# Kernel optimization log

Hardware: AMD Instinct MI355X
Metric: run time of the kernel (lower is better)

## Reference

```python
import jax, jax.numpy as jnp
import numpy as np

N, E, F_IN, H, D, HID, G = 50000, 800000, 64, 4, 32, 128, 1024
NEG_SLOPE = 0.2


def setup_inputs():
    key = jax.random.key(0)
    ks = jax.random.split(key, 32)
    inp = {
        "x": jax.random.normal(ks[0], (N, F_IN), dtype=jnp.float32),
        "edge_index": jax.random.randint(ks[1], (2, E), 0, N, dtype=jnp.int64),
        "batch": jnp.sort(jax.random.randint(ks[2], (N,), 0, G, dtype=jnp.int64)),
    }
    dims = [F_IN, HID, HID]
    i = 3
    for l, din in enumerate(dims):
        s = 1.0 / np.sqrt(din)
        inp[f"Wl{l}"] = jax.random.normal(ks[i], (din, H * D), dtype=jnp.float32) * s; i += 1
        inp[f"bl{l}"] = jnp.zeros((H * D,), dtype=jnp.float32)
        inp[f"Wr{l}"] = jax.random.normal(ks[i], (din, H * D), dtype=jnp.float32) * s; i += 1
        inp[f"br{l}"] = jnp.zeros((H * D,), dtype=jnp.float32)
        inp[f"att{l}"] = jax.random.normal(ks[i], (H, D), dtype=jnp.float32) * (1.0 / np.sqrt(D)); i += 1
        inp[f"b{l}"] = jnp.zeros((H * D,), dtype=jnp.float32)
    inp["Wh"] = jax.random.normal(ks[i], (HID, 1), dtype=jnp.float32) * (1.0 / np.sqrt(HID))
    inp["bh"] = jnp.zeros((1,), dtype=jnp.float32)
    return inp


def gatv2_layer(x, src, dst, Wl, bl, Wr, br, att, b):
    # GATv2Conv (eval mode, no dropout): e_ij = att . leaky_relu(Wl x_j + Wr x_i)
    xl = (x @ Wl + bl).reshape(-1, H, D)   # source transform
    xr = (x @ Wr + br).reshape(-1, H, D)   # target transform
    m = xl[src] + xr[dst]                  # [E,H,D]
    e = jnp.where(m >= 0, m, NEG_SLOPE * m)
    score = jnp.einsum("ehd,hd->eh", e, att)          # [E,H]
    smax = jax.ops.segment_max(score, dst, num_segments=N)  # [N,H]
    expv = jnp.exp(score - smax[dst])
    denom = jax.ops.segment_sum(expv, dst, num_segments=N)
    alpha = expv / denom[dst]                          # softmax over in-edges of dst
    agg = jax.ops.segment_sum(alpha[:, :, None] * xl[src], dst, num_segments=N)
    return agg.reshape(-1, H * D) + b


def reference(x, edge_index, batch, Wl0, bl0, Wr0, br0, att0, b0,
              Wl1, bl1, Wr1, br1, att1, b1,
              Wl2, bl2, Wr2, br2, att2, b2, Wh, bh):
    src, dst = edge_index[0], edge_index[1]
    params = [(Wl0, bl0, Wr0, br0, att0, b0),
              (Wl1, bl1, Wr1, br1, att1, b1),
              (Wl2, bl2, Wr2, br2, att2, b2)]
    h = x
    for p in params:
        h = gatv2_layer(h, src, dst, *p)
        h = jax.nn.elu(h)  # dropout inactive in eval
    # global mean pool over graphs
    sums = jax.ops.segment_sum(h, batch, num_segments=G)
    cnt = jax.ops.segment_sum(jnp.ones((h.shape[0],), h.dtype), batch, num_segments=G)
    pooled = sums / jnp.maximum(cnt, 1.0)[:, None]
    return pooled @ Wh + bh
```

## Files before the change

kernel.cpp:

```cpp
#include <hip/hip_runtime.h>
#include <hip/hip_fp16.h>
#include <math.h>

#define N_NODES 50000
#define N_EDGES 800000
#define HD 128
#define GG 1024
#define NEG_SLOPE 0.2f
#define SCAN_B 1024
#define NB ((N_NODES + SCAN_B - 1) / SCAN_B)

typedef __attribute__((ext_vector_type(8))) short bf16x8;
typedef __attribute__((ext_vector_type(4))) float f32x4;

__device__ __forceinline__ unsigned short f2bf(float v) {
    unsigned u = __float_as_uint(v);
    u += 0x7fff + ((u >> 16) & 1);
    return (unsigned short)(u >> 16);
}
__device__ __forceinline__ float bf2f(unsigned short s) {
    return __uint_as_float((unsigned)s << 16);
}
__device__ __forceinline__ void h8_to_f(const uint4& r, float4& v0, float4& v1) {
    const __half2* h = (const __half2*)&r;
    float2 a = __half22float2(h[0]), b = __half22float2(h[1]);
    float2 c = __half22float2(h[2]), d = __half22float2(h[3]);
    v0 = make_float4(a.x, a.y, b.x, b.y);
    v1 = make_float4(c.x, c.y, d.x, d.y);
}

__global__ void convert_x(const float* __restrict__ x, unsigned short* __restrict__ Xh,
                          unsigned short* __restrict__ Xl, int total)
{
    int i = blockIdx.x * 256 + threadIdx.x;
    if (i >= total) return;
    float v = x[i];
    unsigned short hi = f2bf(v);
    unsigned short lo = f2bf(v - bf2f(hi));
    Xh[i] = hi; Xl[i] = lo;
}

__global__ void convert_w_all(const float* __restrict__ W0l, const float* __restrict__ W0r,
                              const float* __restrict__ W1l, const float* __restrict__ W1r,
                              const float* __restrict__ W2l, const float* __restrict__ W2r,
                              unsigned short* __restrict__ Wth, unsigned short* __restrict__ Wtl)
{
    int t = blockIdx.x * 256 + threadIdx.x;
    if (t >= 256 * 64 + 2 * 256 * 128) return;
    int l, local, K;
    const float* Wl; const float* Wr;
    if (t < 256 * 64)            { l = 0; local = t;              K = 64;  Wl = W0l; Wr = W0r; }
    else if (t < 256 * 64 + 256 * 128) { l = 1; local = t - 256 * 64;  K = 128; Wl = W1l; Wr = W1r; }
    else                         { l = 2; local = t - 256 * 64 - 256 * 128; K = 128; Wl = W2l; Wr = W2r; }
    int c = local / K, k = local - c * K;
    float v = (c < 128) ? Wl[(size_t)k * 128 + c] : Wr[(size_t)k * 128 + (c - 128)];
    unsigned short hi = f2bf(v);
    unsigned short lo = f2bf(v - bf2f(hi));
    Wth[l * 256 * 128 + local] = hi;
    Wtl[l * 256 * 128 + local] = lo;
}

template<int K>
__launch_bounds__(256)
__global__ void gemm_mfma(const unsigned short* __restrict__ Xh, const unsigned short* __restrict__ Xl,
                          const unsigned short* __restrict__ Wth, const unsigned short* __restrict__ Wtl,
                          const float* __restrict__ bl, const float* __restrict__ br,
                          __half* __restrict__ Cl16, float* __restrict__ Cr, int n)
{
    constexpr int NCH = K / 32;
    const int tid  = threadIdx.x;
    const int wave = tid >> 6;
    const int lane = tid & 63;
    const int quad = lane >> 4;
    const int l15  = lane & 15;
    const int row0 = blockIdx.x * 64;

    f32x4 acc[4][4];
    #pragma unroll
    for (int i = 0; i < 4; i++)
        #pragma unroll
        for (int j = 0; j < 4; j++) acc[i][j] = (f32x4){0.f, 0.f, 0.f, 0.f};

    size_t aoff[4];
    #pragma unroll
    for (int mt = 0; mt < 4; mt++) {
        int r = row0 + mt * 16 + l15;
        if (r >= n) r = n - 1;
        aoff[mt] = (size_t)r * K + quad * 8;
    }
    size_t boff[4];
    #pragma unroll
    for (int nt = 0; nt < 4; nt++)
        boff[nt] = (size_t)(wave * 64 + nt * 16 + l15) * K + quad * 8;

    bf16x8 ah[4], al[4], bh[4], bo[4];
    #pragma unroll
    for (int mt = 0; mt < 4; mt++) {
        ah[mt] = *(const bf16x8*)(Xh + aoff[mt]);
        al[mt] = *(const bf16x8*)(Xl + aoff[mt]);
    }
    #pragma unroll
    for (int nt = 0; nt < 4; nt++) {
        bh[nt] = *(const bf16x8*)(Wth + boff[nt]);
        bo[nt] = *(const bf16x8*)(Wtl + boff[nt]);
    }

    #pragma unroll
    for (int ch = 1; ch <= NCH; ch++) {
        bf16x8 nah[4], nal[4], nbh[4], nbo[4];
        if (ch < NCH) {
            const int ko = ch * 32;
            #pragma unroll
            for (int mt = 0; mt < 4; mt++) {
                nah[mt] = *(const bf16x8*)(Xh + aoff[mt] + ko);
                nal[mt] = *(const bf16x8*)(Xl + aoff[mt] + ko);
            }
            #pragma unroll
            for (int nt = 0; nt < 4; nt++) {
                nbh[nt] = *(const bf16x8*)(Wth + boff[nt] + ko);
                nbo[nt] = *(const bf16x8*)(Wtl + boff[nt] + ko);
            }
        }
        #pragma unroll
        for (int nt = 0; nt < 4; nt++) {
            #pragma unroll
            for (int mt = 0; mt < 4; mt++) {
                acc[mt][nt] = __builtin_amdgcn_mfma_f32_16x16x32_bf16(ah[mt], bh[nt], acc[mt][nt], 0, 0, 0);
                acc[mt][nt] = __builtin_amdgcn_mfma_f32_16x16x32_bf16(ah[mt], bo[nt], acc[mt][nt], 0, 0, 0);
                acc[mt][nt] = __builtin_amdgcn_mfma_f32_16x16x32_bf16(al[mt], bh[nt], acc[mt][nt], 0, 0, 0);
            }
        }
        if (ch < NCH) {
            #pragma unroll
            for (int i = 0; i < 4; i++) {
                ah[i] = nah[i]; al[i] = nal[i];
                bh[i] = nbh[i]; bo[i] = nbo[i];
            }
        }
    }

    const bool isL = (wave < 2);
    const int colbase = (wave & 1) * 64;
    const float* bias = isL ? bl : br;
    #pragma unroll
    for (int nt = 0; nt < 4; nt++) {
        const int col = colbase + nt * 16 + l15;
        const float bv = bias[col];
        #pragma unroll
        for (int mt = 0; mt < 4; mt++) {
            #pragma unroll
            for (int r = 0; r < 4; r++) {
                const int row = row0 + mt * 16 + quad * 4 + r;
                if (row < n) {
                    const float v = acc[mt][nt][r] + bv;
                    if (isL) Cl16[(size_t)row * 128 + col] = __float2half_rn(v);
                    else     Cr  [(size_t)row * 128 + col] = v;
                }
            }
        }
    }
}

__global__ void deg_gptr(const int* __restrict__ dst, int* __restrict__ deg,
                         const int* __restrict__ batch, int* __restrict__ gptr)
{
    int i = blockIdx.x * 256 + threadIdx.x;
    if (i < N_EDGES) atomicAdd(&deg[dst[i]], 1);
    if (i <= N_NODES) {
        if (i == 0) {
            for (int g = 0; g <= batch[0]; g++) gptr[g] = 0;
        } else if (i == N_NODES) {
            for (int g = batch[N_NODES - 1] + 1; g <= GG; g++) gptr[g] = N_NODES;
        } else {
            int b0 = batch[i - 1], b1 = batch[i];
            for (int g = b0 + 1; g <= b1; g++) gptr[g] = i;
        }
    }
}

__launch_bounds__(SCAN_B)
__global__ void scan_block(const int* __restrict__ deg, int* __restrict__ rowptr,
                           int* __restrict__ btot)
{
    __shared__ int s[SCAN_B];
    const int tid = threadIdx.x;
    const int i = blockIdx.x * SCAN_B + tid;
    int v = (i < N_NODES) ? deg[i] : 0;
    s[tid] = v;
    __syncthreads();
    for (int off = 1; off < SCAN_B; off <<= 1) {
        int t = (tid >= off) ? s[tid - off] : 0;
        __syncthreads();
        s[tid] += t;
        __syncthreads();
    }
    if (i < N_NODES) rowptr[i] = s[tid] - v;
    if (tid == SCAN_B - 1) btot[blockIdx.x] = s[SCAN_B - 1];
}

__global__ void scan_btot(const int* __restrict__ btot, int* __restrict__ boff) {
    const int t = threadIdx.x;
    int v = (t < NB) ? btot[t] : 0;
    const int orig = v;
    #pragma unroll
    for (int off = 1; off < 64; off <<= 1) {
        int u = __shfl_up(v, off);
        if (t >= off) v += u;
    }
    if (t < NB) boff[t] = v - orig;
    if (t == NB - 1) boff[NB] = v;
}

__global__ void scan_add(const int* __restrict__ boff, int* __restrict__ rowptr,
                         int* __restrict__ cursor)
{
    int i = blockIdx.x * 256 + threadIdx.x;
    if (i < N_NODES) {
        int r = rowptr[i] + boff[i >> 10];
        rowptr[i] = r;
        cursor[i] = r;
    }
    if (i == N_NODES) rowptr[N_NODES] = boff[NB];
}

__global__ void scatter_csr(const int* __restrict__ src, const int* __restrict__ dst,
                            int* __restrict__ cursor, int* __restrict__ csr_src)
{
    int e = blockIdx.x * 256 + threadIdx.x;
    if (e >= N_EDGES) return;
    int pos = atomicAdd(&cursor[dst[e]], 1);
    csr_src[pos] = src[e];
}

__launch_bounds__(256)
__global__ void node_attn(const __half* __restrict__ xl16, const float* __restrict__ xr,
                          const int* __restrict__ rowptr, const int* __restrict__ csr_src,
                          const float* __restrict__ att, const float* __restrict__ bvec,
                          unsigned short* __restrict__ Hh, unsigned short* __restrict__ Hl)
{
    const int node = (blockIdx.x * 256 + threadIdx.x) >> 6;
    const int lane = threadIdx.x & 63;
    if (node >= N_NODES) return;
    const int eslot = lane >> 4;
    const int li    = lane & 15;

    const float* xrp = xr + (size_t)node * HD + li * 8;
    const float4 xr0 = *(const float4*)(xrp);
    const float4 xr1 = *(const float4*)(xrp + 4);
    const float4 aw0 = *(const float4*)(att + li * 8);
    const float4 aw1 = *(const float4*)(att + li * 8 + 4);
    const int beg = rowptr[node];
    const int end = rowptr[node + 1];

    float m = -1e30f, l = 0.f;
    float4 a0 = make_float4(0.f, 0.f, 0.f, 0.f);
    float4 a1 = make_float4(0.f, 0.f, 0.f, 0.f);

    int i0 = beg + eslot;
    int s0 = (i0 < end) ? csr_src[i0] : 0;
    uint4 cur = *(const uint4*)(xl16 + (size_t)s0 * HD + li * 8);

    for (int base = beg; base < end; base += 4) {
        const bool valid = (base + eslot) < end;
        uint4 nxt = cur;
        if (base + 4 < end) {
            int e2 = base + 4 + eslot;
            int s2 = (e2 < end) ? csr_src[e2] : 0;
            nxt = *(const uint4*)(xl16 + (size_t)s2 * HD + li * 8);
        }
        float4 v0, v1;
        h8_to_f(cur, v0, v1);
        float t, p;
        t = v0.x + xr0.x; t = fmaxf(t, NEG_SLOPE * t); p  = t * aw0.x;
        t = v0.y + xr0.y; t = fmaxf(t, NEG_SLOPE * t); p += t * aw0.y;
        t = v0.z + xr0.z; t = fmaxf(t, NEG_SLOPE * t); p += t * aw0.z;
        t = v0.w + xr0.w; t = fmaxf(t, NEG_SLOPE * t); p += t * aw0.w;
        t = v1.x + xr1.x; t = fmaxf(t, NEG_SLOPE * t); p += t * aw1.x;
        t = v1.y + xr1.y; t = fmaxf(t, NEG_SLOPE * t); p += t * aw1.y;
        t = v1.z + xr1.z; t = fmaxf(t, NEG_SLOPE * t); p += t * aw1.z;
        t = v1.w + xr1.w; t = fmaxf(t, NEG_SLOPE * t); p += t * aw1.w;
        p += __shfl_xor(p, 1);
        p += __shfl_xor(p, 2);

        if (!__any(valid && (p > m))) {
            const float w = valid ? __expf(p - m) : 0.f;
            l += w;
            a0.x += w * v0.x; a0.y += w * v0.y; a0.z += w * v0.z; a0.w += w * v0.w;
            a1.x += w * v1.x; a1.y += w * v1.y; a1.z += w * v1.z; a1.w += w * v1.w;
        } else {
            const float mn = valid ? fmaxf(m, p) : m;
            const float sc = __expf(m - mn);
            const float w  = valid ? __expf(p - mn) : 0.f;
            l = l * sc + w;
            a0.x = a0.x * sc + w * v0.x; a0.y = a0.y * sc + w * v0.y;
            a0.z = a0.z * sc + w * v0.z; a0.w = a0.w * sc + w * v0.w;
            a1.x = a1.x * sc + w * v1.x; a1.y = a1.y * sc + w * v1.y;
            a1.z = a1.z * sc + w * v1.z; a1.w = a1.w * sc + w * v1.w;
            m = mn;
        }
        cur = nxt;
    }

    #pragma unroll
    for (int off = 16; off <= 32; off <<= 1) {
        const float mo = __shfl_xor(m, off);
        const float lo = __shfl_xor(l, off);
        float4 b0, b1;
        b0.x = __shfl_xor(a0.x, off); b0.y = __shfl_xor(a0.y, off);
        b0.z = __shfl_xor(a0.z, off); b0.w = __shfl_xor(a0.w, off);
        b1.x = __shfl_xor(a1.x, off); b1.y = __shfl_xor(a1.y, off);
        b1.z = __shfl_xor(a1.z, off); b1.w = __shfl_xor(a1.w, off);
        const float mm = fmaxf(m, mo);
        const float e1 = __expf(m - mm);
        const float e2 = __expf(mo - mm);
        l = l * e1 + lo * e2;
        a0.x = a0.x * e1 + b0.x * e2; a0.y = a0.y * e1 + b0.y * e2;
        a0.z = a0.z * e1 + b0.z * e2; a0.w = a0.w * e1 + b0.w * e2;
        a1.x = a1.x * e1 + b1.x * e2; a1.y = a1.y * e1 + b1.y * e2;
        a1.z = a1.z * e1 + b1.z * e2; a1.w = a1.w * e1 + b1.w * e2;
        m = mm;
    }

    if (eslot == 0) {
        const float inv = (l > 0.f) ? 1.f / l : 0.f;
        const float4 bb0 = *(const float4*)(bvec + li * 8);
        const float4 bb1 = *(const float4*)(bvec + li * 8 + 4);
        float o[8];
        o[0] = a0.x * inv + bb0.x; o[1] = a0.y * inv + bb0.y;
        o[2] = a0.z * inv + bb0.z; o[3] = a0.w * inv + bb0.w;
        o[4] = a1.x * inv + bb1.x; o[5] = a1.y * inv + bb1.y;
        o[6] = a1.z * inv + bb1.z; o[7] = a1.w * inv + bb1.w;
        uint4 ph, pl;
        unsigned* php = (unsigned*)&ph;
        unsigned* plp = (unsigned*)&pl;
        #pragma unroll
        for (int j = 0; j < 4; j++) {
            float u0 = o[2*j], u1 = o[2*j+1];
            u0 = (u0 > 0.f) ? u0 : expm1f(u0);
            u1 = (u1 > 0.f) ? u1 : expm1f(u1);
            unsigned short h0 = f2bf(u0), h1 = f2bf(u1);
            unsigned short q0 = f2bf(u0 - bf2f(h0)), q1 = f2bf(u1 - bf2f(h1));
            php[j] = (unsigned)h0 | ((unsigned)h1 << 16);
            plp[j] = (unsigned)q0 | ((unsigned)q1 << 16);
        }
        *(uint4*)(Hh + (size_t)node * HD + li * 8) = ph;
        *(uint4*)(Hl + (size_t)node * HD + li * 8) = pl;
    }
}

__launch_bounds__(256)
__global__ void pool_head(const unsigned short* __restrict__ Hh, const unsigned short* __restrict__ Hl,
                          const int* __restrict__ gptr, const float* __restrict__ Wh,
                          const float* __restrict__ bh, float* __restrict__ out)
{
    const int g = (blockIdx.x * 256 + threadIdx.x) >> 6;
    const int lane = threadIdx.x & 63;
    if (g >= GG) return;
    const int b0 = gptr[g], b1 = gptr[g + 1];
    const float2 w = *(const float2*)(Wh + lane * 2);
    float sx = 0.f, sy = 0.f;
    for (int i = b0; i < b1; i++) {
        const unsigned vh = *(const unsigned*)(Hh + (size_t)i * HD + lane * 2);
        const unsigned vl = *(const unsigned*)(Hl + (size_t)i * HD + lane * 2);
        sx += bf2f((unsigned short)(vh & 0xffff)) + bf2f((unsigned short)(vl & 0xffff));
        sy += bf2f((unsigned short)(vh >> 16))    + bf2f((unsigned short)(vl >> 16));
    }
    float d = sx * w.x + sy * w.y;
    d += __shfl_xor(d, 1);
    d += __shfl_xor(d, 2);
    d += __shfl_xor(d, 4);
    d += __shfl_xor(d, 8);
    d += __shfl_xor(d, 16);
    d += __shfl_xor(d, 32);
    if (lane == 0) out[g] = d / fmaxf((float)(b1 - b0), 1.f) + bh[0];
}

extern "C" void kernel_launch(void* const* d_in, const int* in_sizes, int n_in,
                              void* d_out, int out_size, void* d_ws, size_t ws_size,
                              hipStream_t stream)
{
    const float* x     = (const float*)d_in[0];
    const int*   edge  = (const int*)d_in[1];
    const int*   batch = (const int*)d_in[2];
    const int*   src   = edge;
    const int*   dst   = edge + N_EDGES;
    const float* Wh    = (const float*)d_in[21];
    const float* bh    = (const float*)d_in[22];
    float* out = (float*)d_out;

    const size_t N128 = (size_t)N_NODES * HD;
    __half* xl16  = (__half*)d_ws;
    float* buf_xr = (float*)(xl16 + N128);
    unsigned short* Xh  = (unsigned short*)(buf_xr + N128);
    unsigned short* Xl_ = Xh + N128;
    unsigned short* Wth = Xl_ + N128;
    unsigned short* Wtl = Wth + 3 * 256 * 128;
    int* deg     = (int*)(Wtl + 3 * 256 * 128);
    int* rowptr  = deg + N_NODES;
    int* cursor  = rowptr + N_NODES + 1;
    int* csr_src = cursor + N_NODES;
    int* btot    = csr_src + N_EDGES;
    int* boff    = btot + NB;
    int* gptr    = boff + NB + 1;

    hipMemsetAsync(deg, 0, (size_t)N_NODES * sizeof(int), stream);
    deg_gptr<<<(N_EDGES + 255) / 256, 256, 0, stream>>>(dst, deg, batch, gptr);
    scan_block<<<NB, SCAN_B, 0, stream>>>(deg, rowptr, btot);
    scan_btot<<<1, 64, 0, stream>>>(btot, boff);
    scan_add<<<(N_NODES + 256) / 256, 256, 0, stream>>>(boff, rowptr, cursor);
    scatter_csr<<<(N_EDGES + 255) / 256, 256, 0, stream>>>(src, dst, cursor, csr_src);

    convert_x<<<(N_NODES * 64 + 255) / 256, 256, 0, stream>>>(x, Xh, Xl_, N_NODES * 64);
    convert_w_all<<<(256 * 64 + 2 * 256 * 128 + 255) / 256, 256, 0, stream>>>(
        (const float*)d_in[3],  (const float*)d_in[5],
        (const float*)d_in[9],  (const float*)d_in[11],
        (const float*)d_in[15], (const float*)d_in[17], Wth, Wtl);

    const int gemm_grid = (N_NODES + 63) / 64;
    const int attn_grid = (N_NODES + 3) / 4;

    for (int l = 0; l < 3; l++) {
        const float* bl  = (const float*)d_in[4 + 6 * l];
        const float* br  = (const float*)d_in[6 + 6 * l];
        const float* att = (const float*)d_in[7 + 6 * l];
        const float* bb  = (const float*)d_in[8 + 6 * l];

        if (l == 0)
            gemm_mfma<64><<<gemm_grid, 256, 0, stream>>>(Xh, Xl_, Wth, Wtl,
                                                         bl, br, xl16, buf_xr, N_NODES);
        else
            gemm_mfma<128><<<gemm_grid, 256, 0, stream>>>(Xh, Xl_,
                                                          Wth + l * 256 * 128, Wtl + l * 256 * 128,
                                                          bl, br, xl16, buf_xr, N_NODES);
        node_attn<<<attn_grid, 256, 0, stream>>>(xl16, buf_xr, rowptr, csr_src,
                                                 att, bb, Xh, Xl_);
    }

    pool_head<<<GG / 4, 256, 0, stream>>>(Xh, Xl_, gptr, Wh, bh, out);
}
```

Baseline: 536.0 us.

## Keep GEMM weights in registers, widen attention edge parallelism, fuse convert kernels

The GEMM now loads each wave's full weight slice into registers once and streams six 16-row A tiles per block (96 rows), prefetching the next tile, with launch bounds set for two blocks per SM. The attention kernel now processes 8 edges per wave with 16 features per lane, using 32-byte gathers, and always does the online-softmax rescale instead of branching on a wave-wide vote. The x and weight conversion kernels are merged into one launch. The GEMM change raises register pressure and may lower occupancy, and the unconditional rescale adds exp work per edge.

```diff
diff --git a/kernel.cpp b/kernel.cpp
--- a/kernel.cpp
+++ b/kernel.cpp
@@ -29,29 +29,30 @@
     v1 = make_float4(c.x, c.y, d.x, d.y);
 }
 
-__global__ void convert_x(const float* __restrict__ x, unsigned short* __restrict__ Xh,
-                          unsigned short* __restrict__ Xl, int total)
-{
-    int i = blockIdx.x * 256 + threadIdx.x;
-    if (i >= total) return;
-    float v = x[i];
-    unsigned short hi = f2bf(v);
-    unsigned short lo = f2bf(v - bf2f(hi));
-    Xh[i] = hi; Xl[i] = lo;
-}
-
-__global__ void convert_w_all(const float* __restrict__ W0l, const float* __restrict__ W0r,
-                              const float* __restrict__ W1l, const float* __restrict__ W1r,
-                              const float* __restrict__ W2l, const float* __restrict__ W2r,
-                              unsigned short* __restrict__ Wth, unsigned short* __restrict__ Wtl)
+#define XTOT (N_NODES * 64)
+#define WTOT (256 * 64 + 2 * 256 * 128)
+__global__ void convert_all(const float* __restrict__ x,
+                            const float* __restrict__ W0l, const float* __restrict__ W0r,
+                            const float* __restrict__ W1l, const float* __restrict__ W1r,
+                            const float* __restrict__ W2l, const float* __restrict__ W2r,
+                            unsigned short* __restrict__ Xh, unsigned short* __restrict__ Xl,
+                            unsigned short* __restrict__ Wth, unsigned short* __restrict__ Wtl)
 {
     int t = blockIdx.x * 256 + threadIdx.x;
-    if (t >= 256 * 64 + 2 * 256 * 128) return;
+    if (t < XTOT) {
+        float v = x[t];
+        unsigned short hi = f2bf(v);
+        unsigned short lo = f2bf(v - bf2f(hi));
+        Xh[t] = hi; Xl[t] = lo;
+        return;
+    }
+    t -= XTOT;
+    if (t >= WTOT) return;
     int l, local, K;
     const float* Wl; const float* Wr;
-    if (t < 256 * 64)            { l = 0; local = t;              K = 64;  Wl = W0l; Wr = W0r; }
-    else if (t < 256 * 64 + 256 * 128) { l = 1; local = t - 256 * 64;  K = 128; Wl = W1l; Wr = W1r; }
-    else                         { l = 2; local = t - 256 * 64 - 256 * 128; K = 128; Wl = W2l; Wr = W2r; }
+    if (t < 256 * 64)                  { l = 0; local = t;                    K = 64;  Wl = W0l; Wr = W0r; }
+    else if (t < 256 * 64 + 256 * 128) { l = 1; local = t - 256 * 64;         K = 128; Wl = W1l; Wr = W1r; }
+    else                               { l = 2; local = t - 256*64 - 256*128; K = 128; Wl = W2l; Wr = W2r; }
     int c = local / K, k = local - c * K;
     float v = (c < 128) ? Wl[(size_t)k * 128 + c] : Wr[(size_t)k * 128 + (c - 128)];
     unsigned short hi = f2bf(v);
@@ -61,102 +62,91 @@
 }
 
 template<int K>
-__launch_bounds__(256)
+__launch_bounds__(256, 2)
 __global__ void gemm_mfma(const unsigned short* __restrict__ Xh, const unsigned short* __restrict__ Xl,
                           const unsigned short* __restrict__ Wth, const unsigned short* __restrict__ Wtl,
                           const float* __restrict__ bl, const float* __restrict__ br,
                           __half* __restrict__ Cl16, float* __restrict__ Cr, int n)
 {
     constexpr int NCH = K / 32;
+    constexpr int MT = 6;
     const int tid  = threadIdx.x;
     const int wave = tid >> 6;
     const int lane = tid & 63;
     const int quad = lane >> 4;
     const int l15  = lane & 15;
-    const int row0 = blockIdx.x * 64;
-
-    f32x4 acc[4][4];
+    const int row0 = blockIdx.x * 96;
+
+    bf16x8 bh[NCH][4], bo[NCH][4];
     #pragma unroll
-    for (int i = 0; i < 4; i++)
-        #pragma unroll
-        for (int j = 0; j < 4; j++) acc[i][j] = (f32x4){0.f, 0.f, 0.f, 0.f};
-
-    size_t aoff[4];
-    #pragma unroll
-    for (int mt = 0; mt < 4; mt++) {
+    for (int ch = 0; ch < NCH; ch++)
+        #pragma unroll
+        for (int nt = 0; nt < 4; nt++) {
+            const size_t wo = (size_t)(wave * 64 + nt * 16 + l15) * K + ch * 32 + quad * 8;
+            bh[ch][nt] = *(const bf16x8*)(Wth + wo);
+            bo[ch][nt] = *(const bf16x8*)(Wtl + wo);
+        }
+
+    auto arow = [&](int mt) -> size_t {
         int r = row0 + mt * 16 + l15;
         if (r >= n) r = n - 1;
-        aoff[mt] = (size_t)r * K + quad * 8;
-    }
-    size_t boff[4];
-    #pragma unroll
-    for (int nt = 0; nt < 4; nt++)
-        boff[nt] = (size_t)(wave * 64 + nt * 16 + l15) * K + quad * 8;
-
-    bf16x8 ah[4], al[4], bh[4], bo[4];
-    #pragma unroll
-    for (int mt = 0; mt < 4; mt++) {
-        ah[mt] = *(const bf16x8*)(Xh + aoff[mt]);
-        al[mt] = *(const bf16x8*)(Xl + aoff[mt]);
-    }
-    #pragma unroll
-    for (int nt = 0; nt < 4; nt++) {
-        bh[nt] = *(const bf16x8*)(Wth + boff[nt]);
-        bo[nt] = *(const bf16x8*)(Wtl + boff[nt]);
-    }
-
-    #pragma unroll
-    for (int ch = 1; ch <= NCH; ch++) {
-        bf16x8 nah[4], nal[4], nbh[4], nbo[4];
-        if (ch < NCH) {
-            const int ko = ch * 32;
-            #pragma unroll
-            for (int mt = 0; mt < 4; mt++) {
-                nah[mt] = *(const bf16x8*)(Xh + aoff[mt] + ko);
-                nal[mt] = *(const bf16x8*)(Xl + aoff[mt] + ko);
-            }
-            #pragma unroll
-            for (int nt = 0; nt < 4; nt++) {
-                nbh[nt] = *(const bf16x8*)(Wth + boff[nt] + ko);
-                nbo[nt] = *(const bf16x8*)(Wtl + boff[nt] + ko);
-            }
-        }
-        #pragma unroll
-        for (int nt = 0; nt < 4; nt++) {
-            #pragma unroll
-            for (int mt = 0; mt < 4; mt++) {
-                acc[mt][nt] = __builtin_amdgcn_mfma_f32_16x16x32_bf16(ah[mt], bh[nt], acc[mt][nt], 0, 0, 0);
-                acc[mt][nt] = __builtin_amdgcn_mfma_f32_16x16x32_bf16(ah[mt], bo[nt], acc[mt][nt], 0, 0, 0);
-                acc[mt][nt] = __builtin_amdgcn_mfma_f32_16x16x32_bf16(al[mt], bh[nt], acc[mt][nt], 0, 0, 0);
-            }
-        }
-        if (ch < NCH) {
-            #pragma unroll
-            for (int i = 0; i < 4; i++) {
-                ah[i] = nah[i]; al[i] = nal[i];
-                bh[i] = nbh[i]; bo[i] = nbo[i];
-            }
+        return (size_t)r * K + quad * 8;
+    };
+
+    bf16x8 ah[NCH], al[NCH], nah[NCH], nal[NCH];
+    {
+        const size_t ao = arow(0);
+        #pragma unroll
+        for (int ch = 0; ch < NCH; ch++) {
+            ah[ch] = *(const bf16x8*)(Xh + ao + ch * 32);
+            al[ch] = *(const bf16x8*)(Xl + ao + ch * 32);
         }
     }
 
     const bool isL = (wave < 2);
     const int colbase = (wave & 1) * 64;
     const float* bias = isL ? bl : br;
+    float bv[4];
     #pragma unroll
-    for (int nt = 0; nt < 4; nt++) {
-        const int col = colbase + nt * 16 + l15;
-        const float bv = bias[col];
-        #pragma unroll
-        for (int mt = 0; mt < 4; mt++) {
+    for (int nt = 0; nt < 4; nt++) bv[nt] = bias[colbase + nt * 16 + l15];
+
+    #pragma unroll
+    for (int mt = 0; mt < MT; mt++) {
+        if (mt + 1 < MT) {
+            const size_t ao = arow(mt + 1);
+            #pragma unroll
+            for (int ch = 0; ch < NCH; ch++) {
+                nah[ch] = *(const bf16x8*)(Xh + ao + ch * 32);
+                nal[ch] = *(const bf16x8*)(Xl + ao + ch * 32);
+            }
+        }
+        f32x4 acc[4];
+        #pragma unroll
+        for (int nt = 0; nt < 4; nt++) acc[nt] = (f32x4){0.f, 0.f, 0.f, 0.f};
+        #pragma unroll
+        for (int ch = 0; ch < NCH; ch++)
+            #pragma unroll
+            for (int nt = 0; nt < 4; nt++) {
+                acc[nt] = __builtin_amdgcn_mfma_f32_16x16x32_bf16(ah[ch], bh[ch][nt], acc[nt], 0, 0, 0);
+                acc[nt] = __builtin_amdgcn_mfma_f32_16x16x32_bf16(ah[ch], bo[ch][nt], acc[nt], 0, 0, 0);
+                acc[nt] = __builtin_amdgcn_mfma_f32_16x16x32_bf16(al[ch], bh[ch][nt], acc[nt], 0, 0, 0);
+            }
+        #pragma unroll
+        for (int nt = 0; nt < 4; nt++) {
+            const int col = colbase + nt * 16 + l15;
             #pragma unroll
             for (int r = 0; r < 4; r++) {
                 const int row = row0 + mt * 16 + quad * 4 + r;
                 if (row < n) {
-                    const float v = acc[mt][nt][r] + bv;
+                    const float v = acc[nt][r] + bv[nt];
                     if (isL) Cl16[(size_t)row * 128 + col] = __float2half_rn(v);
                     else     Cr  [(size_t)row * 128 + col] = v;
                 }
             }
+        }
+        if (mt + 1 < MT) {
+            #pragma unroll
+            for (int ch = 0; ch < NCH; ch++) { ah[ch] = nah[ch]; al[ch] = nal[ch]; }
         }
     }
 }
@@ -241,35 +231,41 @@
     const int node = (blockIdx.x * 256 + threadIdx.x) >> 6;
     const int lane = threadIdx.x & 63;
     if (node >= N_NODES) return;
-    const int eslot = lane >> 4;
-    const int li    = lane & 15;
-
-    const float* xrp = xr + (size_t)node * HD + li * 8;
-    const float4 xr0 = *(const float4*)(xrp);
+    const int eslot = lane >> 3;
+    const int lj    = lane & 7;
+
+    const float* xrp = xr + (size_t)node * HD + lj * 16;
+    const float4 xr0 = *(const float4*)(xrp + 0);
     const float4 xr1 = *(const float4*)(xrp + 4);
-    const float4 aw0 = *(const float4*)(att + li * 8);
-    const float4 aw1 = *(const float4*)(att + li * 8 + 4);
+    const float4 xr2 = *(const float4*)(xrp + 8);
+    const float4 xr3 = *(const float4*)(xrp + 12);
+    const float4 aw0 = *(const float4*)(att + lj * 16 + 0);
+    const float4 aw1 = *(const float4*)(att + lj * 16 + 4);
+    const float4 aw2 = *(const float4*)(att + lj * 16 + 8);
+    const float4 aw3 = *(const float4*)(att + lj * 16 + 12);
     const int beg = rowptr[node];
     const int end = rowptr[node + 1];
 
     float m = -1e30f, l = 0.f;
-    float4 a0 = make_float4(0.f, 0.f, 0.f, 0.f);
-    float4 a1 = make_float4(0.f, 0.f, 0.f, 0.f);
+    float4 A0 = {0,0,0,0}, A1 = {0,0,0,0}, A2 = {0,0,0,0}, A3 = {0,0,0,0};
 
     int i0 = beg + eslot;
     int s0 = (i0 < end) ? csr_src[i0] : 0;
-    uint4 cur = *(const uint4*)(xl16 + (size_t)s0 * HD + li * 8);
-
-    for (int base = beg; base < end; base += 4) {
+    const uint4* rp = (const uint4*)(xl16 + (size_t)s0 * HD + lj * 16);
+    uint4 c0 = rp[0], c1 = rp[1];
+
+    for (int base = beg; base < end; base += 8) {
         const bool valid = (base + eslot) < end;
-        uint4 nxt = cur;
-        if (base + 4 < end) {
-            int e2 = base + 4 + eslot;
+        uint4 n0 = c0, n1 = c1;
+        if (base + 8 < end) {
+            int e2 = base + 8 + eslot;
             int s2 = (e2 < end) ? csr_src[e2] : 0;
-            nxt = *(const uint4*)(xl16 + (size_t)s2 * HD + li * 8);
-        }
-        float4 v0, v1;
-        h8_to_f(cur, v0, v1);
+            const uint4* np = (const uint4*)(xl16 + (size_t)s2 * HD + lj * 16);
+            n0 = np[0]; n1 = np[1];
+        }
+        float4 v0, v1, v2, v3;
+        h8_to_f(c0, v0, v1);
+        h8_to_f(c1, v2, v3);
         float t, p;
         t = v0.x + xr0.x; t = fmaxf(t, NEG_SLOPE * t); p  = t * aw0.x;
         t = v0.y + xr0.y; t = fmaxf(t, NEG_SLOPE * t); p += t * aw0.y;
@@ -279,63 +275,76 @@
         t = v1.y + xr1.y; t = fmaxf(t, NEG_SLOPE * t); p += t * aw1.y;
         t = v1.z + xr1.z; t = fmaxf(t, NEG_SLOPE * t); p += t * aw1.z;
         t = v1.w + xr1.w; t = fmaxf(t, NEG_SLOPE * t); p += t * aw1.w;
+        t = v2.x + xr2.x; t = fmaxf(t, NEG_SLOPE * t); p += t * aw2.x;
+        t = v2.y + xr2.y; t = fmaxf(t, NEG_SLOPE * t); p += t * aw2.y;
+        t = v2.z + xr2.z; t = fmaxf(t, NEG_SLOPE * t); p += t * aw2.z;
+        t = v2.w + xr2.w; t = fmaxf(t, NEG_SLOPE * t); p += t * aw2.w;
+        t = v3.x + xr3.x; t = fmaxf(t, NEG_SLOPE * t); p += t * aw3.x;
+        t = v3.y + xr3.y; t = fmaxf(t, NEG_SLOPE * t); p += t * aw3.y;
+        t = v3.z + xr3.z; t = fmaxf(t, NEG_SLOPE * t); p += t * aw3.z;
+        t = v3.w + xr3.w; t = fmaxf(t, NEG_SLOPE * t); p += t * aw3.w;
         p += __shfl_xor(p, 1);
-        p += __shfl_xor(p, 2);
-
-        if (!__any(valid && (p > m))) {
-            const float w = valid ? __expf(p - m) : 0.f;
-            l += w;
-            a0.x += w * v0.x; a0.y += w * v0.y; a0.z += w * v0.z; a0.w += w * v0.w;
-            a1.x += w * v1.x; a1.y += w * v1.y; a1.z += w * v1.z; a1.w += w * v1.w;
-        } else {
-            const float mn = valid ? fmaxf(m, p) : m;
-            const float sc = __expf(m - mn);
-            const float w  = valid ? __expf(p - mn) : 0.f;
-            l = l * sc + w;
-            a0.x = a0.x * sc + w * v0.x; a0.y = a0.y * sc + w * v0.y;
-            a0.z = a0.z * sc + w * v0.z; a0.w = a0.w * sc + w * v0.w;
-            a1.x = a1.x * sc + w * v1.x; a1.y = a1.y * sc + w * v1.y;
-            a1.z = a1.z * sc + w * v1.z; a1.w = a1.w * sc + w * v1.w;
-            m = mn;
-        }
-        cur = nxt;
+
+        const float pe = valid ? p : -1e30f;
+        const float mn = fmaxf(m, pe);
+        const float sc = __expf(m - mn);
+        const float w  = valid ? __expf(p - mn) : 0.f;
+        l = l * sc + w;
+        A0.x = A0.x * sc + w * v0.x; A0.y = A0.y * sc + w * v0.y;
+        A0.z = A0.z * sc + w * v0.z; A0.w = A0.w * sc + w * v0.w;
+        A1.x = A1.x * sc + w * v1.x; A1.y = A1.y * sc + w * v1.y;
+        A1.z = A1.z * sc + w * v1.z; A1.w = A1.w * sc + w * v1.w;
+        A2.x = A2.x * sc + w * v2.x; A2.y = A2.y * sc + w * v2.y;
+        A2.z = A2.z * sc + w * v2.z; A2.w = A2.w * sc + w * v2.w;
+        A3.x = A3.x * sc + w * v3.x; A3.y = A3.y * sc + w * v3.y;
+        A3.z = A3.z * sc + w * v3.z; A3.w = A3.w * sc + w * v3.w;
+        m = mn;
+        c0 = n0; c1 = n1;
     }
 
     #pragma unroll
-    for (int off = 16; off <= 32; off <<= 1) {
+    for (int off = 8; off <= 32; off <<= 1) {
         const float mo = __shfl_xor(m, off);
         const float lo = __shfl_xor(l, off);
-        float4 b0, b1;
-        b0.x = __shfl_xor(a0.x, off); b0.y = __shfl_xor(a0.y, off);
-        b0.z = __shfl_xor(a0.z, off); b0.w = __shfl_xor(a0.w, off);
-        b1.x = __shfl_xor(a1.x, off); b1.y = __shfl_xor(a1.y, off);
-        b1.z = __shfl_xor(a1.z, off); b1.w = __shfl_xor(a1.w, off);
+        float4 B0, B1, B2, B3;
+        B0.x = __shfl_xor(A0.x, off); B0.y = __shfl_xor(A0.y, off);
+        B0.z = __shfl_xor(A0.z, off); B0.w = __shfl_xor(A0.w, off);
+        B1.x = __shfl_xor(A1.x, off); B1.y = __shfl_xor(A1.y, off);
+        B1.z = __shfl_xor(A1.z, off); B1.w = __shfl_xor(A1.w, off);
+        B2.x = __shfl_xor(A2.x, off); B2.y = __shfl_xor(A2.y, off);
+        B2.z = __shfl_xor(A2.z, off); B2.w = __shfl_xor(A2.w, off);
+        B3.x = __shfl_xor(A3.x, off); B3.y = __shfl_xor(A3.y, off);
+        B3.z = __shfl_xor(A3.z, off); B3.w = __shfl_xor(A3.w, off);
         const float mm = fmaxf(m, mo);
         const float e1 = __expf(m - mm);
         const float e2 = __expf(mo - mm);
         l = l * e1 + lo * e2;
-        a0.x = a0.x * e1 + b0.x * e2; a0.y = a0.y * e1 + b0.y * e2;
-        a0.z = a0.z * e1 + b0.z * e2; a0.w = a0.w * e1 + b0.w * e2;
-        a1.x = a1.x * e1 + b1.x * e2; a1.y = a1.y * e1 + b1.y * e2;
-        a1.z = a1.z * e1 + b1.z * e2; a1.w = a1.w * e1 + b1.w * e2;
+        A0.x = A0.x * e1 + B0.x * e2; A0.y = A0.y * e1 + B0.y * e2;
+        A0.z = A0.z * e1 + B0.z * e2; A0.w = A0.w * e1 + B0.w * e2;
+        A1.x = A1.x * e1 + B1.x * e2; A1.y = A1.y * e1 + B1.y * e2;
+        A1.z = A1.z * e1 + B1.z * e2; A1.w = A1.w * e1 + B1.w * e2;
+        A2.x = A2.x * e1 + B2.x * e2; A2.y = A2.y * e1 + B2.y * e2;
+        A2.z = A2.z * e1 + B2.z * e2; A2.w = A2.w * e1 + B2.w * e2;
+        A3.x = A3.x * e1 + B3.x * e2; A3.y = A3.y * e1 + B3.y * e2;
+        A3.z = A3.z * e1 + B3.z * e2; A3.w = A3.w * e1 + B3.w * e2;
         m = mm;
     }
 
     if (eslot == 0) {
         const float inv = (l > 0.f) ? 1.f / l : 0.f;
-        const float4 bb0 = *(const float4*)(bvec + li * 8);
-        const float4 bb1 = *(const float4*)(bvec + li * 8 + 4);
-        float o[8];
-        o[0] = a0.x * inv + bb0.x; o[1] = a0.y * inv + bb0.y;
-        o[2] = a0.z * inv + bb0.z; o[3] = a0.w * inv + bb0.w;
-        o[4] = a1.x * inv + bb1.x; o[5] = a1.y * inv + bb1.y;
-        o[6] = a1.z * inv + bb1.z; o[7] = a1.w * inv + bb1.w;
-        uint4 ph, pl;
-        unsigned* php = (unsigned*)&ph;
-        unsigned* plp = (unsigned*)&pl;
-        #pragma unroll
-        for (int j = 0; j < 4; j++) {
-            float u0 = o[2*j], u1 = o[2*j+1];
+        float o[16];
+        const float* bb = bvec + lj * 16;
+        o[0]=A0.x; o[1]=A0.y; o[2]=A0.z; o[3]=A0.w;
+        o[4]=A1.x; o[5]=A1.y; o[6]=A1.z; o[7]=A1.w;
+        o[8]=A2.x; o[9]=A2.y; o[10]=A2.z; o[11]=A2.w;
+        o[12]=A3.x; o[13]=A3.y; o[14]=A3.z; o[15]=A3.w;
+        uint4 ph[2], pl[2];
+        unsigned* php = (unsigned*)ph;
+        unsigned* plp = (unsigned*)pl;
+        #pragma unroll
+        for (int j = 0; j < 8; j++) {
+            float u0 = o[2*j]   * inv + bb[2*j];
+            float u1 = o[2*j+1] * inv + bb[2*j+1];
             u0 = (u0 > 0.f) ? u0 : expm1f(u0);
             u1 = (u1 > 0.f) ? u1 : expm1f(u1);
             unsigned short h0 = f2bf(u0), h1 = f2bf(u1);
@@ -343,8 +352,10 @@
             php[j] = (unsigned)h0 | ((unsigned)h1 << 16);
             plp[j] = (unsigned)q0 | ((unsigned)q1 << 16);
         }
-        *(uint4*)(Hh + (size_t)node * HD + li * 8) = ph;
-        *(uint4*)(Hl + (size_t)node * HD + li * 8) = pl;
+        uint4* hp = (uint4*)(Hh + (size_t)node * HD + lj * 16);
+        uint4* lp = (uint4*)(Hl + (size_t)node * HD + lj * 16);
+        hp[0] = ph[0]; hp[1] = ph[1];
+        lp[0] = pl[0]; lp[1] = pl[1];
     }
 }
 
@@ -410,13 +421,14 @@
     scan_add<<<(N_NODES + 256) / 256, 256, 0, stream>>>(boff, rowptr, cursor);
     scatter_csr<<<(N_EDGES + 255) / 256, 256, 0, stream>>>(src, dst, cursor, csr_src);
 
-    convert_x<<<(N_NODES * 64 + 255) / 256, 256, 0, stream>>>(x, Xh, Xl_, N_NODES * 64);
-    convert_w_all<<<(256 * 64 + 2 * 256 * 128 + 255) / 256, 256, 0, stream>>>(
+    convert_all<<<(XTOT + WTOT + 255) / 256, 256, 0, stream>>>(
+        x,
         (const float*)d_in[3],  (const float*)d_in[5],
         (const float*)d_in[9],  (const float*)d_in[11],
-        (const float*)d_in[15], (const float*)d_in[17], Wth, Wtl);
-
-    const int gemm_grid = (N_NODES + 63) / 64;
+        (const float*)d_in[15], (const float*)d_in[17],
+        Xh, Xl_, Wth, Wtl);
+
+    const int gemm_grid = (N_NODES + 95) / 96;
     const int attn_grid = (N_NODES + 3) / 4;
 
     for (int l = 0; l < 3; l++) {
```

Result: slower. 635.1 us (+18.5%).

## Fuse preprocessing into cooperative kernel, store xr as fp16, restructure GEMM tiling

Applied to the files above, without the earlier changes.

Merges the CSR build, scan, and the x and weight bf16 split conversions into a single cooperative kernel that uses grid syncs, replacing seven launches and a memset. The GEMM now keeps the whole weight slice in registers and walks 6 row tiles of 96 rows per block with register prefetch, under launch_bounds(256,2). The target-transform output xr is stored in fp16 instead of fp32, which halves its write and read traffic but reduces its precision. The cooperative kernel runs on only 256 blocks and serializes its phases with grid syncs, which may leave the atomic-heavy phases underused.

```diff
diff --git a/kernel.cpp b/kernel.cpp
--- a/kernel.cpp
+++ b/kernel.cpp
@@ -1,5 +1,6 @@
 #include <hip/hip_runtime.h>
 #include <hip/hip_fp16.h>
+#include <hip/hip_cooperative_groups.h>
 #include <math.h>
 
 #define N_NODES 50000
@@ -7,8 +8,9 @@
 #define HD 128
 #define GG 1024
 #define NEG_SLOPE 0.2f
-#define SCAN_B 1024
-#define NB ((N_NODES + SCAN_B - 1) / SCAN_B)
+#define XTOT (N_NODES * 64)
+#define WTOT (256 * 64 + 2 * 256 * 128)
+#define NCHUNKS ((N_NODES + 255) / 256)
 
 typedef __attribute__((ext_vector_type(8))) short bf16x8;
 typedef __attribute__((ext_vector_type(4))) float f32x4;
@@ -29,144 +31,45 @@
     v1 = make_float4(c.x, c.y, d.x, d.y);
 }
 
-__global__ void convert_x(const float* __restrict__ x, unsigned short* __restrict__ Xh,
-                          unsigned short* __restrict__ Xl, int total)
+__global__ void preprocess(const int* __restrict__ src, const int* __restrict__ dst,
+                           const int* __restrict__ batch, const float* __restrict__ x,
+                           const float* __restrict__ W0l, const float* __restrict__ W0r,
+                           const float* __restrict__ W1l, const float* __restrict__ W1r,
+                           const float* __restrict__ W2l, const float* __restrict__ W2r,
+                           int* __restrict__ deg, int* __restrict__ rowptr,
+                           int* __restrict__ cursor, int* __restrict__ csr_src,
+                           int* __restrict__ gptr, int* __restrict__ bsum,
+                           unsigned short* __restrict__ Xh, unsigned short* __restrict__ Xl,
+                           unsigned short* __restrict__ Wth, unsigned short* __restrict__ Wtl)
 {
-    int i = blockIdx.x * 256 + threadIdx.x;
-    if (i >= total) return;
-    float v = x[i];
-    unsigned short hi = f2bf(v);
-    unsigned short lo = f2bf(v - bf2f(hi));
-    Xh[i] = hi; Xl[i] = lo;
-}
-
-__global__ void convert_w_all(const float* __restrict__ W0l, const float* __restrict__ W0r,
-                              const float* __restrict__ W1l, const float* __restrict__ W1r,
-                              const float* __restrict__ W2l, const float* __restrict__ W2r,
-                              unsigned short* __restrict__ Wth, unsigned short* __restrict__ Wtl)
-{
-    int t = blockIdx.x * 256 + threadIdx.x;
-    if (t >= 256 * 64 + 2 * 256 * 128) return;
-    int l, local, K;
-    const float* Wl; const float* Wr;
-    if (t < 256 * 64)            { l = 0; local = t;              K = 64;  Wl = W0l; Wr = W0r; }
-    else if (t < 256 * 64 + 256 * 128) { l = 1; local = t - 256 * 64;  K = 128; Wl = W1l; Wr = W1r; }
-    else                         { l = 2; local = t - 256 * 64 - 256 * 128; K = 128; Wl = W2l; Wr = W2r; }
-    int c = local / K, k = local - c * K;
-    float v = (c < 128) ? Wl[(size_t)k * 128 + c] : Wr[(size_t)k * 128 + (c - 128)];
-    unsigned short hi = f2bf(v);
-    unsigned short lo = f2bf(v - bf2f(hi));
-    Wth[l * 256 * 128 + local] = hi;
-    Wtl[l * 256 * 128 + local] = lo;
-}
-
-template<int K>
-__launch_bounds__(256)
-__global__ void gemm_mfma(const unsigned short* __restrict__ Xh, const unsigned short* __restrict__ Xl,
-                          const unsigned short* __restrict__ Wth, const unsigned short* __restrict__ Wtl,
-                          const float* __restrict__ bl, const float* __restrict__ br,
-                          __half* __restrict__ Cl16, float* __restrict__ Cr, int n)
-{
-    constexpr int NCH = K / 32;
+    cooperative_groups::grid_group grid = cooperative_groups::this_grid();
     const int tid  = threadIdx.x;
-    const int wave = tid >> 6;
-    const int lane = tid & 63;
-    const int quad = lane >> 4;
-    const int l15  = lane & 15;
-    const int row0 = blockIdx.x * 64;
-
-    f32x4 acc[4][4];
-    #pragma unroll
-    for (int i = 0; i < 4; i++)
-        #pragma unroll
-        for (int j = 0; j < 4; j++) acc[i][j] = (f32x4){0.f, 0.f, 0.f, 0.f};
-
-    size_t aoff[4];
-    #pragma unroll
-    for (int mt = 0; mt < 4; mt++) {
-        int r = row0 + mt * 16 + l15;
-        if (r >= n) r = n - 1;
-        aoff[mt] = (size_t)r * K + quad * 8;
-    }
-    size_t boff[4];
-    #pragma unroll
-    for (int nt = 0; nt < 4; nt++)
-        boff[nt] = (size_t)(wave * 64 + nt * 16 + l15) * K + quad * 8;
-
-    bf16x8 ah[4], al[4], bh[4], bo[4];
-    #pragma unroll
-    for (int mt = 0; mt < 4; mt++) {
-        ah[mt] = *(const bf16x8*)(Xh + aoff[mt]);
-        al[mt] = *(const bf16x8*)(Xl + aoff[mt]);
-    }
-    #pragma unroll
-    for (int nt = 0; nt < 4; nt++) {
-        bh[nt] = *(const bf16x8*)(Wth + boff[nt]);
-        bo[nt] = *(const bf16x8*)(Wtl + boff[nt]);
-    }
-
-    #pragma unroll
-    for (int ch = 1; ch <= NCH; ch++) {
-        bf16x8 nah[4], nal[4], nbh[4], nbo[4];
-        if (ch < NCH) {
-            const int ko = ch * 32;
-            #pragma unroll
-            for (int mt = 0; mt < 4; mt++) {
-                nah[mt] = *(const bf16x8*)(Xh + aoff[mt] + ko);
-                nal[mt] = *(const bf16x8*)(Xl + aoff[mt] + ko);
-            }
-            #pragma unroll
-            for (int nt = 0; nt < 4; nt++) {
-                nbh[nt] = *(const bf16x8*)(Wth + boff[nt] + ko);
-                nbo[nt] = *(const bf16x8*)(Wtl + boff[nt] + ko);
-            }
-        }
-        #pragma unroll
-        for (int nt = 0; nt < 4; nt++) {
-            #pragma unroll
-            for (int mt = 0; mt < 4; mt++) {
-                acc[mt][nt] = __builtin_amdgcn_mfma_f32_16x16x32_bf16(ah[mt], bh[nt], acc[mt][nt], 0, 0, 0);
-                acc[mt][nt] = __builtin_amdgcn_mfma_f32_16x16x32_bf16(ah[mt], bo[nt], acc[mt][nt], 0, 0, 0);
-                acc[mt][nt] = __builtin_amdgcn_mfma_f32_16x16x32_bf16(al[mt], bh[nt], acc[mt][nt], 0, 0, 0);
-            }
-        }
-        if (ch < NCH) {
-            #pragma unroll
-            for (int i = 0; i < 4; i++) {
-                ah[i] = nah[i]; al[i] = nal[i];
-                bh[i] = nbh[i]; bo[i] = nbo[i];
-            }
-        }
-    }
-
-    const bool isL = (wave < 2);
-    const int colbase = (wave & 1) * 64;
-    const float* bias = isL ? bl : br;
-    #pragma unroll
-    for (int nt = 0; nt < 4; nt++) {
-        const int col = colbase + nt * 16 + l15;
-        const float bv = bias[col];
-        #pragma unroll
-        for (int mt = 0; mt < 4; mt++) {
-            #pragma unroll
-            for (int r = 0; r < 4; r++) {
-                const int row = row0 + mt * 16 + quad * 4 + r;
-                if (row < n) {
-                    const float v = acc[mt][nt][r] + bv;
-                    if (isL) Cl16[(size_t)row * 128 + col] = __float2half_rn(v);
-                    else     Cr  [(size_t)row * 128 + col] = v;
-                }
-            }
-        }
-    }
-}
-
-__global__ void deg_gptr(const int* __restrict__ dst, int* __restrict__ deg,
-                         const int* __restrict__ batch, int* __restrict__ gptr)
-{
-    int i = blockIdx.x * 256 + threadIdx.x;
-    if (i < N_EDGES) atomicAdd(&deg[dst[i]], 1);
-    if (i <= N_NODES) {
+    const int gtid = blockIdx.x * 256 + tid;
+    const int gsz  = gridDim.x * 256;
+    __shared__ int s[256];
+
+    for (int i = gtid; i < N_NODES; i += gsz) deg[i] = 0;
+    for (int i = gtid; i < XTOT; i += gsz) {
+        float v = x[i];
+        unsigned short hi = f2bf(v);
+        Xh[i] = hi; Xl[i] = f2bf(v - bf2f(hi));
+    }
+    for (int t0 = gtid; t0 < WTOT; t0 += gsz) {
+        int t = t0, l, local, K;
+        const float* Wl; const float* Wr;
+        if (t < 256 * 64)                  { l = 0; local = t;                    K = 64;  Wl = W0l; Wr = W0r; }
+        else if (t < 256 * 64 + 256 * 128) { l = 1; local = t - 256 * 64;         K = 128; Wl = W1l; Wr = W1r; }
+        else                               { l = 2; local = t - 256*64 - 256*128; K = 128; Wl = W2l; Wr = W2r; }
+        int c = local / K, k = local - c * K;
+        float v = (c < 128) ? Wl[(size_t)k * 128 + c] : Wr[(size_t)k * 128 + (c - 128)];
+        unsigned short hi = f2bf(v);
+        Wth[l * 256 * 128 + local] = hi;
+        Wtl[l * 256 * 128 + local] = f2bf(v - bf2f(hi));
+    }
+    grid.sync();
+
+    for (int e = gtid; e < N_EDGES; e += gsz) atomicAdd(&deg[dst[e]], 1);
+    for (int i = gtid; i <= N_NODES; i += gsz) {
         if (i == 0) {
             for (int g = 0; g <= batch[0]; g++) gptr[g] = 0;
         } else if (i == N_NODES) {
@@ -176,64 +79,145 @@
             for (int g = b0 + 1; g <= b1; g++) gptr[g] = i;
         }
     }
-}
-
-__launch_bounds__(SCAN_B)
-__global__ void scan_block(const int* __restrict__ deg, int* __restrict__ rowptr,
-                           int* __restrict__ btot)
-{
-    __shared__ int s[SCAN_B];
-    const int tid = threadIdx.x;
-    const int i = blockIdx.x * SCAN_B + tid;
-    int v = (i < N_NODES) ? deg[i] : 0;
-    s[tid] = v;
-    __syncthreads();
-    for (int off = 1; off < SCAN_B; off <<= 1) {
-        int t = (tid >= off) ? s[tid - off] : 0;
+    grid.sync();
+
+    for (int c = blockIdx.x; c < NCHUNKS; c += gridDim.x) {
+        const int i = c * 256 + tid;
+        int v = (i < N_NODES) ? deg[i] : 0;
+        s[tid] = v;
         __syncthreads();
-        s[tid] += t;
+        #pragma unroll
+        for (int off = 1; off < 256; off <<= 1) {
+            int t = (tid >= off) ? s[tid - off] : 0;
+            __syncthreads();
+            s[tid] += t;
+            __syncthreads();
+        }
+        if (i < N_NODES) rowptr[i] = s[tid] - v;
+        if (tid == 255) bsum[c] = s[255];
         __syncthreads();
     }
-    if (i < N_NODES) rowptr[i] = s[tid] - v;
-    if (tid == SCAN_B - 1) btot[blockIdx.x] = s[SCAN_B - 1];
-}
-
-__global__ void scan_btot(const int* __restrict__ btot, int* __restrict__ boff) {
-    const int t = threadIdx.x;
-    int v = (t < NB) ? btot[t] : 0;
-    const int orig = v;
-    #pragma unroll
-    for (int off = 1; off < 64; off <<= 1) {
-        int u = __shfl_up(v, off);
-        if (t >= off) v += u;
-    }
-    if (t < NB) boff[t] = v - orig;
-    if (t == NB - 1) boff[NB] = v;
-}
-
-__global__ void scan_add(const int* __restrict__ boff, int* __restrict__ rowptr,
-                         int* __restrict__ cursor)
-{
-    int i = blockIdx.x * 256 + threadIdx.x;
-    if (i < N_NODES) {
-        int r = rowptr[i] + boff[i >> 10];
+    grid.sync();
+
+    if (blockIdx.x == 0) {
+        int v = (tid < NCHUNKS) ? bsum[tid] : 0;
+        s[tid] = v;
+        __syncthreads();
+        #pragma unroll
+        for (int off = 1; off < 256; off <<= 1) {
+            int t = (tid >= off) ? s[tid - off] : 0;
+            __syncthreads();
+            s[tid] += t;
+            __syncthreads();
+        }
+        if (tid < NCHUNKS) bsum[tid] = s[tid] - v;
+        if (tid == 0) rowptr[N_NODES] = s[255];
+    }
+    grid.sync();
+
+    for (int i = gtid; i < N_NODES; i += gsz) {
+        int r = rowptr[i] + bsum[i >> 8];
         rowptr[i] = r;
         cursor[i] = r;
     }
-    if (i == N_NODES) rowptr[N_NODES] = boff[NB];
-}
-
-__global__ void scatter_csr(const int* __restrict__ src, const int* __restrict__ dst,
-                            int* __restrict__ cursor, int* __restrict__ csr_src)
+    grid.sync();
+
+    for (int e = gtid; e < N_EDGES; e += gsz) {
+        int pos = atomicAdd(&cursor[dst[e]], 1);
+        csr_src[pos] = src[e];
+    }
+}
+
+template<int K>
+__launch_bounds__(256, 2)
+__global__ void gemm_mfma(const unsigned short* __restrict__ Xh, const unsigned short* __restrict__ Xl,
+                          const unsigned short* __restrict__ Wth, const unsigned short* __restrict__ Wtl,
+                          const float* __restrict__ bl, const float* __restrict__ br,
+                          __half* __restrict__ Cl16, __half* __restrict__ Cr16, int n)
 {
-    int e = blockIdx.x * 256 + threadIdx.x;
-    if (e >= N_EDGES) return;
-    int pos = atomicAdd(&cursor[dst[e]], 1);
-    csr_src[pos] = src[e];
+    constexpr int NCH = K / 32;
+    constexpr int MT = 6;
+    const int tid  = threadIdx.x;
+    const int wave = tid >> 6;
+    const int lane = tid & 63;
+    const int quad = lane >> 4;
+    const int l15  = lane & 15;
+    const int row0 = blockIdx.x * 96;
+
+    bf16x8 bh[NCH][4], bo[NCH][4];
+    #pragma unroll
+    for (int ch = 0; ch < NCH; ch++)
+        #pragma unroll
+        for (int nt = 0; nt < 4; nt++) {
+            const size_t wo = (size_t)(wave * 64 + nt * 16 + l15) * K + ch * 32 + quad * 8;
+            bh[ch][nt] = *(const bf16x8*)(Wth + wo);
+            bo[ch][nt] = *(const bf16x8*)(Wtl + wo);
+        }
+
+    auto arow = [&](int mt) -> size_t {
+        int r = row0 + mt * 16 + l15;
+        if (r >= n) r = n - 1;
+        return (size_t)r * K + quad * 8;
+    };
+
+    bf16x8 ah[NCH], al[NCH], nah[NCH], nal[NCH];
+    {
+        const size_t ao = arow(0);
+        #pragma unroll
+        for (int ch = 0; ch < NCH; ch++) {
+            ah[ch] = *(const bf16x8*)(Xh + ao + ch * 32);
+            al[ch] = *(const bf16x8*)(Xl + ao + ch * 32);
+        }
+    }
+
+    const bool isL = (wave < 2);
+    const int colbase = (wave & 1) * 64;
+    const float* bias = isL ? bl : br;
+    __half* C = isL ? Cl16 : Cr16;
+    float bv[4];
+    #pragma unroll
+    for (int nt = 0; nt < 4; nt++) bv[nt] = bias[colbase + nt * 16 + l15];
+
+    #pragma unroll
+    for (int mt = 0; mt < MT; mt++) {
+        if (mt + 1 < MT) {
+            const size_t ao = arow(mt + 1);
+            #pragma unroll
+            for (int ch = 0; ch < NCH; ch++) {
+                nah[ch] = *(const bf16x8*)(Xh + ao + ch * 32);
+                nal[ch] = *(const bf16x8*)(Xl + ao + ch * 32);
+            }
+        }
+        f32x4 acc[4];
+        #pragma unroll
+        for (int nt = 0; nt < 4; nt++) acc[nt] = (f32x4){0.f, 0.f, 0.f, 0.f};
+        #pragma unroll
+        for (int ch = 0; ch < NCH; ch++)
+            #pragma unroll
+            for (int nt = 0; nt < 4; nt++) {
+                acc[nt] = __builtin_amdgcn_mfma_f32_16x16x32_bf16(ah[ch], bh[ch][nt], acc[nt], 0, 0, 0);
+                acc[nt] = __builtin_amdgcn_mfma_f32_16x16x32_bf16(ah[ch], bo[ch][nt], acc[nt], 0, 0, 0);
+                acc[nt] = __builtin_amdgcn_mfma_f32_16x16x32_bf16(al[ch], bh[ch][nt], acc[nt], 0, 0, 0);
+            }
+        #pragma unroll
+        for (int nt = 0; nt < 4; nt++) {
+            const int col = colbase + nt * 16 + l15;
+            #pragma unroll
+            for (int r = 0; r < 4; r++) {
+                const int row = row0 + mt * 16 + quad * 4 + r;
+                if (row < n)
+                    C[(size_t)row * 128 + col] = __float2half_rn(acc[nt][r] + bv[nt]);
+            }
+        }
+        if (mt + 1 < MT) {
+            #pragma unroll
+            for (int ch = 0; ch < NCH; ch++) { ah[ch] = nah[ch]; al[ch] = nal[ch]; }
+        }
+    }
 }
 
 __launch_bounds__(256)
-__global__ void node_attn(const __half* __restrict__ xl16, const float* __restrict__ xr,
+__global__ void node_attn(const __half* __restrict__ xl16, const __half* __restrict__ xr16,
                           const int* __restrict__ rowptr, const int* __restrict__ csr_src,
                           const float* __restrict__ att, const float* __restrict__ bvec,
                           unsigned short* __restrict__ Hh, unsigned short* __restrict__ Hl)
@@ -244,9 +228,11 @@
     const int eslot = lane >> 4;
     const int li    = lane & 15;
 
-    const float* xrp = xr + (size_t)node * HD + li * 8;
-    const float4 xr0 = *(const float4*)(xrp);
-    const float4 xr1 = *(const float4*)(xrp + 4);
+    float4 xr0, xr1;
+    {
+        const uint4 xrp = *(const uint4*)(xr16 + (size_t)node * HD + li * 8);
+        h8_to_f(xrp, xr0, xr1);
+    }
     const float4 aw0 = *(const float4*)(att + li * 8);
     const float4 aw1 = *(const float4*)(att + li * 8 + 4);
     const int beg = rowptr[node];
@@ -390,8 +376,8 @@
 
     const size_t N128 = (size_t)N_NODES * HD;
     __half* xl16  = (__half*)d_ws;
-    float* buf_xr = (float*)(xl16 + N128);
-    unsigned short* Xh  = (unsigned short*)(buf_xr + N128);
+    __half* xr16  = xl16 + N128;
+    unsigned short* Xh  = (unsigned short*)(xr16 + N128);
     unsigned short* Xl_ = Xh + N128;
     unsigned short* Wth = Xl_ + N128;
     unsigned short* Wtl = Wth + 3 * 256 * 128;
@@ -399,24 +385,29 @@
     int* rowptr  = deg + N_NODES;
     int* cursor  = rowptr + N_NODES + 1;
     int* csr_src = cursor + N_NODES;
-    int* btot    = csr_src + N_EDGES;
-    int* boff    = btot + NB;
-    int* gptr    = boff + NB + 1;
-
-    hipMemsetAsync(deg, 0, (size_t)N_NODES * sizeof(int), stream);
-    deg_gptr<<<(N_EDGES + 255) / 256, 256, 0, stream>>>(dst, deg, batch, gptr);
-    scan_block<<<NB, SCAN_B, 0, stream>>>(deg, rowptr, btot);
-    scan_btot<<<1, 64, 0, stream>>>(btot, boff);
-    scan_add<<<(N_NODES + 256) / 256, 256, 0, stream>>>(boff, rowptr, cursor);
-    scatter_csr<<<(N_EDGES + 255) / 256, 256, 0, stream>>>(src, dst, cursor, csr_src);
-
-    convert_x<<<(N_NODES * 64 + 255) / 256, 256, 0, stream>>>(x, Xh, Xl_, N_NODES * 64);
-    convert_w_all<<<(256 * 64 + 2 * 256 * 128 + 255) / 256, 256, 0, stream>>>(
-        (const float*)d_in[3],  (const float*)d_in[5],
-        (const float*)d_in[9],  (const float*)d_in[11],
-        (const float*)d_in[15], (const float*)d_in[17], Wth, Wtl);
-
-    const int gemm_grid = (N_NODES + 63) / 64;
+    int* bsum    = csr_src + N_EDGES;
+    int* gptr    = bsum + 256;
+
+    {
+        const float* W0l = (const float*)d_in[3];
+        const float* W0r = (const float*)d_in[5];
+        const float* W1l = (const float*)d_in[9];
+        const float* W1r = (const float*)d_in[11];
+        const float* W2l = (const float*)d_in[15];
+        const float* W2r = (const float*)d_in[17];
+        void* args[] = {
+            (void*)&src, (void*)&dst, (void*)&batch, (void*)&x,
+            (void*)&W0l, (void*)&W0r, (void*)&W1l, (void*)&W1r,
+            (void*)&W2l, (void*)&W2r,
+            (void*)&deg, (void*)&rowptr, (void*)&cursor, (void*)&csr_src,
+            (void*)&gptr, (void*)&bsum,
+            (void*)&Xh, (void*)&Xl_, (void*)&Wth, (void*)&Wtl
+        };
+        hipLaunchCooperativeKernel((const void*)preprocess, dim3(256), dim3(256),
+                                   args, 0, stream);
+    }
+
+    const int gemm_grid = (N_NODES + 95) / 96;
     const int attn_grid = (N_NODES + 3) / 4;
 
     for (int l = 0; l < 3; l++) {
@@ -427,12 +418,12 @@
 
         if (l == 0)
             gemm_mfma<64><<<gemm_grid, 256, 0, stream>>>(Xh, Xl_, Wth, Wtl,
-                                                         bl, br, xl16, buf_xr, N_NODES);
+                                                         bl, br, xl16, xr16, N_NODES);
         else
             gemm_mfma<128><<<gemm_grid, 256, 0, stream>>>(Xh, Xl_,
                                                           Wth + l * 256 * 128, Wtl + l * 256 * 128,
-                                                          bl, br, xl16, buf_xr, N_NODES);
-        node_attn<<<attn_grid, 256, 0, stream>>>(xl16, buf_xr, rowptr, csr_src,
+                                                          bl, br, xl16, xr16, N_NODES);
+        node_attn<<<attn_grid, 256, 0, stream>>>(xl16, xr16, rowptr, csr_src,
                                                  att, bb, Xh, Xl_);
     }
 
```

Measured after the change: 660.0 us. 1.23x slower.
